# Kernel tuning notes

Hardware: AMD Instinct MI355X
Metric: run time of the kernel (lower is better)

The kernel has to match this reference:

```python
import jax, jax.numpy as jnp
import numpy as np

B, T, D = 4, 2048, 1024
N_HEADS = 16
D_HEAD = D // N_HEADS


def setup_inputs() -> dict:
    key = jax.random.key(0)
    ks = jax.random.split(key, 5)
    s = 1.0 / np.sqrt(D)
    return {
        "x": jax.random.normal(ks[0], (B, T, D), dtype=jnp.float32),
        "wq": jax.random.normal(ks[1], (D, D), dtype=jnp.float32) * s,
        "wk": jax.random.normal(ks[2], (D, D), dtype=jnp.float32) * s,
        "wv": jax.random.normal(ks[3], (D, D), dtype=jnp.float32) * s,
        "wo": jax.random.normal(ks[4], (D, D), dtype=jnp.float32) * s,
    }


def reference(x, wq, wk, wv, wo):
    # nn.Linear applies y = x @ W^T (no bias)
    b, t, c = x.shape
    def heads(w):
        return (x @ w.T).reshape(b, t, N_HEADS, D_HEAD).transpose(0, 2, 1, 3)  # (B,H,T,d)
    q, k, v = heads(wq), heads(wk), heads(wv)
    scale = 1.0 / np.sqrt(D_HEAD).astype(np.float32)
    att = jnp.einsum('bhqd,bhkd->bhqk', q, k) * scale
    causal = jnp.tril(jnp.ones((t, t), dtype=bool))
    att = jnp.where(causal[None, None], att, -jnp.inf)
    att = jax.nn.softmax(att, axis=-1)
    # dropout is identity in eval / p acts as 0 for the deterministic reference
    y = jnp.einsum('bhqk,bhkd->bhqd', att, v)
    y = y.transpose(0, 2, 1, 3).reshape(b, t, c)
    return y @ wo.T
```

## Files before the change

### kernel.cpp

```cpp
#include <hip/hip_runtime.h>

#define B_ 4
#define T_ 2048
#define D_ 1024
#define H_ 16
#define DH_ 64
#define M_ (B_*T_)
#define KP 72

typedef __attribute__((ext_vector_type(8))) short short8;
typedef __attribute__((ext_vector_type(4))) float f32x4;
typedef __attribute__((ext_vector_type(4))) unsigned short u16x4;
typedef _Float16 half4f __attribute__((ext_vector_type(4)));

__device__ __forceinline__ unsigned short f2bf(float f) {
  unsigned int u = __float_as_uint(f);
  u += 0x7FFFu + ((u >> 16) & 1u);
  return (unsigned short)(u >> 16);
}

__device__ __forceinline__ void async_copy16(const void* g, void* l) {
  __builtin_amdgcn_global_load_lds(
      (const __attribute__((address_space(1))) unsigned int*)(g),
      (__attribute__((address_space(3))) unsigned int*)(l),
      16, 0, 0);
}

__device__ __forceinline__ f32x4 mfma32(short8 a, short8 b, f32x4 c) {
  return __builtin_amdgcn_mfma_f32_16x16x32_bf16(a, b, c, 0, 0, 0);
}

#define NX4 (M_*D_/4)
#define NW4 (D_*D_/4)
__global__ __launch_bounds__(256) void cvt_all(
    const float* __restrict__ x,  const float* __restrict__ wq,
    const float* __restrict__ wk, const float* __restrict__ wv,
    const float* __restrict__ wo, unsigned short* __restrict__ xb,
    unsigned short* __restrict__ wqb, unsigned short* __restrict__ wkb,
    unsigned short* __restrict__ wvb, unsigned short* __restrict__ wob) {
  int i = blockIdx.x * 256 + threadIdx.x;
  const float* src; unsigned short* dst; int off;
  if (i < NX4)             { src = x;  dst = xb;  off = i; }
  else if (i < NX4 + NW4)  { src = wq; dst = wqb; off = i - NX4; }
  else if (i < NX4 + 2*NW4){ src = wk; dst = wkb; off = i - NX4 - NW4; }
  else if (i < NX4 + 3*NW4){ src = wv; dst = wvb; off = i - NX4 - 2*NW4; }
  else                     { src = wo; dst = wob; off = i - NX4 - 3*NW4; }
  const float4 v = reinterpret_cast<const float4*>(src)[off];
  u16x4 o;
  o.x = f2bf(v.x); o.y = f2bf(v.y); o.z = f2bf(v.z); o.w = f2bf(v.w);
  reinterpret_cast<u16x4*>(dst)[off] = o;
}

__global__ __launch_bounds__(256) void gemm_qkv(
    const unsigned short* __restrict__ A,
    const unsigned short* __restrict__ Wq,
    const unsigned short* __restrict__ Wk,
    const unsigned short* __restrict__ Wv,
    unsigned short* __restrict__ Qo,
    unsigned short* __restrict__ Ko,
    _Float16* __restrict__ Vo) {
  __shared__ __align__(16) unsigned short ldsA[128*32];
  __shared__ __align__(16) unsigned short ldsB[128*32];
  const int tid = threadIdx.x;
  const int w = tid >> 6, lane = tid & 63;
  const int quad = lane >> 4, l16 = lane & 15;
  const int wr = (w >> 1) * 64, wc = (w & 1) * 64;
  const int m0 = blockIdx.x * 128;
  const int seg = blockIdx.y >> 3;
  const int n0 = (blockIdx.y & 7) * 128;
  const unsigned short* Bt = (seg == 0) ? Wq : ((seg == 1) ? Wk : Wv);

  const unsigned short* gA = A  + (size_t)(m0 + w*32 + (lane >> 2)) * D_ + (lane & 3) * 8;
  const unsigned short* gB = Bt + (size_t)(n0 + w*32 + (lane >> 2)) * D_ + (lane & 3) * 8;
  unsigned short* lA = ldsA + (w*32)*32;
  unsigned short* lB = ldsB + (w*32)*32;

  f32x4 acc[4][4] = {};

  for (int k0 = 0; k0 < D_; k0 += 32) {
    __syncthreads();
#pragma unroll
    for (int g = 0; g < 2; ++g) {
      async_copy16(gA + (size_t)k0 + (size_t)g*16*D_, lA + g*16*32);
      async_copy16(gB + (size_t)k0 + (size_t)g*16*D_, lB + g*16*32);
    }
    __syncthreads();
    short8 af[4], bfr[4];
#pragma unroll
    for (int t = 0; t < 4; ++t) {
      af[t]  = *reinterpret_cast<const short8*>(ldsA + (wr + t*16 + l16)*32 + quad*8);
      bfr[t] = *reinterpret_cast<const short8*>(ldsB + (wc + t*16 + l16)*32 + quad*8);
    }
#pragma unroll
    for (int i = 0; i < 4; ++i)
#pragma unroll
      for (int j = 0; j < 4; ++j)
        acc[i][j] = mfma32(af[i], bfr[j], acc[i][j]);
  }

#pragma unroll
  for (int i = 0; i < 4; ++i) {
#pragma unroll
    for (int j = 0; j < 4; ++j) {
      if (seg == 2) {
        const int colc = n0 + wc + j*16 + l16;
        const int hh = colc >> 6, dd = colc & (DH_ - 1);
        const int row0 = m0 + wr + i*16 + quad*4;
        const int bb = row0 >> 11, t0 = row0 & (T_ - 1);
        half4f vh = {(_Float16)acc[i][j][0], (_Float16)acc[i][j][1],
                     (_Float16)acc[i][j][2], (_Float16)acc[i][j][3]};
        *reinterpret_cast<half4f*>(
            &Vo[(size_t)((bb*H_ + hh)*DH_ + dd)*T_ + t0]) = vh;
      } else {
        unsigned short* out = (seg == 0) ? Qo : Ko;
        const float scl = (seg == 0) ? (0.125f * 1.44269504089f) : 1.f;
#pragma unroll
        for (int r = 0; r < 4; ++r) {
          const int row = m0 + wr + i*16 + quad*4 + r;
          const int col = n0 + wc + j*16 + l16;
          out[(size_t)row * D_ + col] = f2bf(acc[i][j][r] * scl);
        }
      }
    }
  }
}

__global__ __launch_bounds__(256) void gemm_out(
    const unsigned short* __restrict__ A,
    const unsigned short* __restrict__ Bt,
    float* __restrict__ Cout) {
  __shared__ __align__(16) unsigned short ldsA[128*32];
  __shared__ __align__(16) unsigned short ldsB[128*32];
  const int tid = threadIdx.x;
  const int w = tid >> 6, lane = tid & 63;
  const int quad = lane >> 4, l16 = lane & 15;
  const int wr = (w >> 1) * 64, wc = (w & 1) * 64;
  const int m0 = blockIdx.x * 128, n0 = blockIdx.y * 128;

  const unsigned short* gA = A  + (size_t)(m0 + w*32 + (lane >> 2)) * D_ + (lane & 3) * 8;
  const unsigned short* gB = Bt + (size_t)(n0 + w*32 + (lane >> 2)) * D_ + (lane & 3) * 8;
  unsigned short* lA = ldsA + (w*32)*32;
  unsigned short* lB = ldsB + (w*32)*32;

  f32x4 acc[4][4] = {};
  for (int k0 = 0; k0 < D_; k0 += 32) {
    __syncthreads();
#pragma unroll
    for (int g = 0; g < 2; ++g) {
      async_copy16(gA + (size_t)k0 + (size_t)g*16*D_, lA + g*16*32);
      async_copy16(gB + (size_t)k0 + (size_t)g*16*D_, lB + g*16*32);
    }
    __syncthreads();
    short8 af[4], bfr[4];
#pragma unroll
    for (int t = 0; t < 4; ++t) {
      af[t]  = *reinterpret_cast<const short8*>(ldsA + (wr + t*16 + l16)*32 + quad*8);
      bfr[t] = *reinterpret_cast<const short8*>(ldsB + (wc + t*16 + l16)*32 + quad*8);
    }
#pragma unroll
    for (int i = 0; i < 4; ++i)
#pragma unroll
      for (int j = 0; j < 4; ++j)
        acc[i][j] = mfma32(af[i], bfr[j], acc[i][j]);
  }
#pragma unroll
  for (int i = 0; i < 4; ++i)
#pragma unroll
    for (int j = 0; j < 4; ++j)
#pragma unroll
      for (int r = 0; r < 4; ++r)
        Cout[(size_t)(m0 + wr + i*16 + quad*4 + r) * D_ + n0 + wc + j*16 + l16] =
            acc[i][j][r];
}

__global__ __launch_bounds__(256) void flash_attn(
    const unsigned short* __restrict__ Q,
    const unsigned short* __restrict__ K,
    const _Float16* __restrict__ Vt,
    unsigned short* __restrict__ Y) {
  __shared__ __align__(16) unsigned short Kl[2][64*KP];
  __shared__ __align__(16) _Float16      Vl[2][64*KP];
  const int bh = blockIdx.x, px = blockIdx.y;
  const int h = bh & (H_ - 1), b = bh >> 4;
  const int tid = threadIdx.x;
  const int w = tid >> 6, lane = tid & 63, quad = lane >> 4, l16 = lane & 15;
  const int hc = h * DH_;

  const int sr = tid >> 2, sc = tid & 3;
  const unsigned short* Kg0 = K + ((size_t)(b*T_) + sr) * D_ + hc + sc*16;
  const _Float16*       Vg0 = Vt + ((size_t)bh * DH_ + sr) * T_ + sc*16;

  uint4 kr0, kr1, vr0, vr1;
  auto loadKV = [&](int kt) {
    const unsigned short* kg = Kg0 + (size_t)kt * 64 * D_;
    const _Float16*       vg = Vg0 + kt * 64;
    kr0 = *reinterpret_cast<const uint4*>(kg);
    kr1 = *reinterpret_cast<const uint4*>(kg + 8);
    vr0 = *reinterpret_cast<const uint4*>(vg);
    vr1 = *reinterpret_cast<const uint4*>(vg + 8);
  };
  auto writeKV = [&](int bi) {
    *reinterpret_cast<uint4*>(&Kl[bi][sr*KP + sc*16])     = kr0;
    *reinterpret_cast<uint4*>(&Kl[bi][sr*KP + sc*16 + 8]) = kr1;
    *reinterpret_cast<uint4*>(&Vl[bi][sr*KP + sc*16])     = vr0;
    *reinterpret_cast<uint4*>(&Vl[bi][sr*KP + sc*16 + 8]) = vr1;
  };

#pragma unroll
  for (int pi = 0; pi < 2; ++pi) {
    const int it = pi ? (31 - px) : px;
    const int qg0 = it*64 + w*16;

    short8 bq[2];
#pragma unroll
    for (int ks = 0; ks < 2; ++ks)
      bq[ks] = *reinterpret_cast<const short8*>(
          Q + (size_t)(b*T_ + qg0 + l16) * D_ + hc + ks*32 + quad*8);

    f32x4 o[4] = {};
    float rs = 0.f;
    const int ktmax = it;

    __syncthreads();
    loadKV(0);
    writeKV(0);
    __syncthreads();

    for (int kt = 0; kt <= ktmax; ++kt) {
      const int cur = kt & 1;
      if (kt < ktmax) loadKV(kt + 1);
      const bool diag = (kt == ktmax);
      const int smax = diag ? w : 3;
      const int diagS = diag ? w : -1;
      for (int s = 0; s <= smax; ++s) {
        const short8 ka0 = *reinterpret_cast<const short8*>(
            &Kl[cur][(s*16 + l16)*KP + quad*8]);
        const short8 ka1 = *reinterpret_cast<const short8*>(
            &Kl[cur][(s*16 + l16)*KP + 32 + quad*8]);
        f32x4 z = {0.f, 0.f, 0.f, 0.f};
        z = mfma32(ka0, bq[0], z);
        z = mfma32(ka1, bq[1], z);
        float p[4];
        const bool dsub = (s == diagS);
#pragma unroll
        for (int r = 0; r < 4; ++r) {
          float pv = __builtin_amdgcn_exp2f(z[r]);
          if (dsub && (quad*4 + r > l16)) pv = 0.f;
          p[r] = pv;
          rs += pv;
        }
        const half4f pf = {(_Float16)p[0], (_Float16)p[1],
                           (_Float16)p[2], (_Float16)p[3]};
#pragma unroll
        for (int dt = 0; dt < 4; ++dt) {
          const half4f vf = *reinterpret_cast<const half4f*>(
              &Vl[cur][(dt*16 + l16)*KP + s*16 + quad*4]);
          o[dt] = __builtin_amdgcn_mfma_f32_16x16x16f16(vf, pf, o[dt], 0, 0, 0);
        }
      }
      if (kt < ktmax) {
        __syncthreads();
        writeKV(cur ^ 1);
        __syncthreads();
      }
    }

    float rt = rs;
    rt += __shfl_xor(rt, 16);
    rt += __shfl_xor(rt, 32);
    const float inv = 1.f / rt;

#pragma unroll
    for (int dt = 0; dt < 4; ++dt) {
      u16x4 yo;
      yo.x = f2bf(o[dt][0] * inv);
      yo.y = f2bf(o[dt][1] * inv);
      yo.z = f2bf(o[dt][2] * inv);
      yo.w = f2bf(o[dt][3] * inv);
      *reinterpret_cast<u16x4*>(
          &Y[(size_t)(b*T_ + qg0 + l16) * D_ + hc + dt*16 + quad*4]) = yo;
    }
  }
}

extern "C" void kernel_launch(void* const* d_in, const int* in_sizes, int n_in,
                              void* d_out, int out_size, void* d_ws, size_t ws_size,
                              hipStream_t stream) {
  const float* x  = (const float*)d_in[0];
  const float* wq = (const float*)d_in[1];
  const float* wk = (const float*)d_in[2];
  const float* wv = (const float*)d_in[3];
  const float* wo = (const float*)d_in[4];

  unsigned short* xb  = (unsigned short*)d_ws;
  unsigned short* wqb = xb  + (size_t)M_ * D_;
  unsigned short* wkb = wqb + (size_t)D_ * D_;
  unsigned short* wvb = wkb + (size_t)D_ * D_;
  unsigned short* wob = wvb + (size_t)D_ * D_;
  unsigned short* q   = wob + (size_t)D_ * D_;
  unsigned short* k   = q   + (size_t)M_ * D_;
  _Float16*       vt  = (_Float16*)(k + (size_t)M_ * D_);
  unsigned short* y   = (unsigned short*)(vt + (size_t)M_ * D_);

  const int ncv = (NX4 + 4*NW4 + 255) / 256;
  cvt_all<<<ncv, 256, 0, stream>>>(x, wq, wk, wv, wo, xb, wqb, wkb, wvb, wob);

  gemm_qkv<<<dim3(M_ / 128, 24), 256, 0, stream>>>(xb, wqb, wkb, wvb, q, k, vt);

  flash_attn<<<dim3(64, 16), 256, 0, stream>>>(q, k, vt, y);

  gemm_out<<<dim3(M_ / 128, D_ / 128), 256, 0, stream>>>(y, wob, (float*)d_out);
}
```

Before: 252.5 us.

## Process both paired query tiles in one KV sweep sharing K/V loads

After: 245.1 us. 2.9% less time.

```diff
diff --git a/kernel.cpp b/kernel.cpp
--- a/kernel.cpp
+++ b/kernel.cpp
@@ -12,6 +12,7 @@
 typedef __attribute__((ext_vector_type(4))) float f32x4;
 typedef __attribute__((ext_vector_type(4))) unsigned short u16x4;
 typedef _Float16 half4f __attribute__((ext_vector_type(4)));
+typedef __fp16 h2raw __attribute__((ext_vector_type(2)));
 
 __device__ __forceinline__ unsigned short f2bf(float f) {
   unsigned int u = __float_as_uint(f);
@@ -28,6 +29,9 @@
 
 __device__ __forceinline__ f32x4 mfma32(short8 a, short8 b, f32x4 c) {
   return __builtin_amdgcn_mfma_f32_16x16x32_bf16(a, b, c, 0, 0, 0);
+}
+__device__ __forceinline__ f32x4 mfma16h(half4f a, half4f b, f32x4 c) {
+  return __builtin_amdgcn_mfma_f32_16x16x16f16(a, b, c, 0, 0, 0);
 }
 
 #define NX4 (M_*D_/4)
@@ -173,7 +177,31 @@
             acc[i][j][r];
 }
 
-__global__ __launch_bounds__(256) void flash_attn(
+__device__ __forceinline__ half4f score_exp(short8 ka0, short8 ka1,
+                                            short8 bq0, short8 bq1,
+                                            bool dmask, int kvb, int qrel,
+                                            f32x4* osum, half4f vones) {
+  f32x4 z = {0.f, 0.f, 0.f, 0.f};
+  z = mfma32(ka0, bq0, z);
+  z = mfma32(ka1, bq1, z);
+  float p0 = __builtin_amdgcn_exp2f(z[0]);
+  float p1 = __builtin_amdgcn_exp2f(z[1]);
+  float p2 = __builtin_amdgcn_exp2f(z[2]);
+  float p3 = __builtin_amdgcn_exp2f(z[3]);
+  if (dmask) {
+    if (kvb + 0 > qrel) p0 = 0.f;
+    if (kvb + 1 > qrel) p1 = 0.f;
+    if (kvb + 2 > qrel) p2 = 0.f;
+    if (kvb + 3 > qrel) p3 = 0.f;
+  }
+  union { h2raw h2[2]; half4f h4; } u;
+  u.h2[0] = __builtin_amdgcn_cvt_pkrtz(p0, p1);
+  u.h2[1] = __builtin_amdgcn_cvt_pkrtz(p2, p3);
+  *osum = mfma16h(vones, u.h4, *osum);
+  return u.h4;
+}
+
+__global__ __launch_bounds__(256, 4) void flash_attn(
     const unsigned short* __restrict__ Q,
     const unsigned short* __restrict__ K,
     const _Float16* __restrict__ Vt,
@@ -185,6 +213,9 @@
   const int tid = threadIdx.x;
   const int w = tid >> 6, lane = tid & 63, quad = lane >> 4, l16 = lane & 15;
   const int hc = h * DH_;
+  const int itA = px, itB = 31 - px;
+  const int qgA = itA*64 + w*16, qgB = itB*64 + w*16;
+  const int ktmax = itB;
 
   const int sr = tid >> 2, sc = tid & 3;
   const unsigned short* Kg0 = K + ((size_t)(b*T_) + sr) * D_ + hc + sc*16;
@@ -206,80 +237,69 @@
     *reinterpret_cast<uint4*>(&Vl[bi][sr*KP + sc*16 + 8]) = vr1;
   };
 
-#pragma unroll
-  for (int pi = 0; pi < 2; ++pi) {
-    const int it = pi ? (31 - px) : px;
-    const int qg0 = it*64 + w*16;
-
-    short8 bq[2];
-#pragma unroll
-    for (int ks = 0; ks < 2; ++ks)
-      bq[ks] = *reinterpret_cast<const short8*>(
-          Q + (size_t)(b*T_ + qg0 + l16) * D_ + hc + ks*32 + quad*8);
-
-    f32x4 o[4] = {};
-    float rs = 0.f;
-    const int ktmax = it;
-
-    __syncthreads();
-    loadKV(0);
-    writeKV(0);
-    __syncthreads();
-
-    for (int kt = 0; kt <= ktmax; ++kt) {
-      const int cur = kt & 1;
-      if (kt < ktmax) loadKV(kt + 1);
-      const bool diag = (kt == ktmax);
-      const int smax = diag ? w : 3;
-      const int diagS = diag ? w : -1;
-      for (int s = 0; s <= smax; ++s) {
-        const short8 ka0 = *reinterpret_cast<const short8*>(
-            &Kl[cur][(s*16 + l16)*KP + quad*8]);
-        const short8 ka1 = *reinterpret_cast<const short8*>(
-            &Kl[cur][(s*16 + l16)*KP + 32 + quad*8]);
-        f32x4 z = {0.f, 0.f, 0.f, 0.f};
-        z = mfma32(ka0, bq[0], z);
-        z = mfma32(ka1, bq[1], z);
-        float p[4];
-        const bool dsub = (s == diagS);
-#pragma unroll
-        for (int r = 0; r < 4; ++r) {
-          float pv = __builtin_amdgcn_exp2f(z[r]);
-          if (dsub && (quad*4 + r > l16)) pv = 0.f;
-          p[r] = pv;
-          rs += pv;
-        }
-        const half4f pf = {(_Float16)p[0], (_Float16)p[1],
-                           (_Float16)p[2], (_Float16)p[3]};
-#pragma unroll
-        for (int dt = 0; dt < 4; ++dt) {
-          const half4f vf = *reinterpret_cast<const half4f*>(
-              &Vl[cur][(dt*16 + l16)*KP + s*16 + quad*4]);
-          o[dt] = __builtin_amdgcn_mfma_f32_16x16x16f16(vf, pf, o[dt], 0, 0, 0);
-        }
+  short8 bqA0, bqA1, bqB0, bqB1;
+  bqA0 = *reinterpret_cast<const short8*>(
+      Q + (size_t)(b*T_ + qgA + l16) * D_ + hc + quad*8);
+  bqA1 = *reinterpret_cast<const short8*>(
+      Q + (size_t)(b*T_ + qgA + l16) * D_ + hc + 32 + quad*8);
+  bqB0 = *reinterpret_cast<const short8*>(
+      Q + (size_t)(b*T_ + qgB + l16) * D_ + hc + quad*8);
+  bqB1 = *reinterpret_cast<const short8*>(
+      Q + (size_t)(b*T_ + qgB + l16) * D_ + hc + 32 + quad*8);
+
+  f32x4 oA[4] = {}, oB[4] = {};
+  f32x4 osA = {}, osB = {};
+  const half4f vones = {(_Float16)1.f, (_Float16)1.f, (_Float16)1.f, (_Float16)1.f};
+  const int qrelW = w*16 + l16;
+
+  loadKV(0);
+  writeKV(0);
+  __syncthreads();
+
+  for (int kt = 0; kt <= ktmax; ++kt) {
+    const int cur = kt & 1;
+    if (kt < ktmax) loadKV(kt + 1);
+    const bool aOn   = (kt <= px);
+    const bool aDiag = (kt == px);
+    const bool bDiag = (kt == ktmax);
+    const int smax = bDiag ? w : 3;
+    for (int s = 0; s <= smax; ++s) {
+      const short8 ka0 = *reinterpret_cast<const short8*>(
+          &Kl[cur][(s*16 + l16)*KP + quad*8]);
+      const short8 ka1 = *reinterpret_cast<const short8*>(
+          &Kl[cur][(s*16 + l16)*KP + 32 + quad*8]);
+      const int kvb = s*16 + quad*4;
+      half4f pfA;
+      if (aOn) pfA = score_exp(ka0, ka1, bqA0, bqA1, aDiag, kvb, qrelW, &osA, vones);
+      const half4f pfB = score_exp(ka0, ka1, bqB0, bqB1, bDiag, kvb, qrelW, &osB, vones);
+#pragma unroll
+      for (int dt = 0; dt < 4; ++dt) {
+        const half4f vf = *reinterpret_cast<const half4f*>(
+            &Vl[cur][(dt*16 + l16)*KP + s*16 + quad*4]);
+        if (aOn) oA[dt] = mfma16h(vf, pfA, oA[dt]);
+        oB[dt] = mfma16h(vf, pfB, oB[dt]);
       }
-      if (kt < ktmax) {
-        __syncthreads();
-        writeKV(cur ^ 1);
-        __syncthreads();
-      }
-    }
-
-    float rt = rs;
-    rt += __shfl_xor(rt, 16);
-    rt += __shfl_xor(rt, 32);
-    const float inv = 1.f / rt;
-
-#pragma unroll
-    for (int dt = 0; dt < 4; ++dt) {
-      u16x4 yo;
-      yo.x = f2bf(o[dt][0] * inv);
-      yo.y = f2bf(o[dt][1] * inv);
-      yo.z = f2bf(o[dt][2] * inv);
-      yo.w = f2bf(o[dt][3] * inv);
-      *reinterpret_cast<u16x4*>(
-          &Y[(size_t)(b*T_ + qg0 + l16) * D_ + hc + dt*16 + quad*4]) = yo;
-    }
+    }
+    if (kt < ktmax) {
+      __syncthreads();
+      writeKV(cur ^ 1);
+      __syncthreads();
+    }
+  }
+
+  const float invA = 1.f / osA[0];
+  const float invB = 1.f / osB[0];
+#pragma unroll
+  for (int dt = 0; dt < 4; ++dt) {
+    u16x4 ya, yb;
+    ya.x = f2bf(oA[dt][0] * invA); ya.y = f2bf(oA[dt][1] * invA);
+    ya.z = f2bf(oA[dt][2] * invA); ya.w = f2bf(oA[dt][3] * invA);
+    yb.x = f2bf(oB[dt][0] * invB); yb.y = f2bf(oB[dt][1] * invB);
+    yb.z = f2bf(oB[dt][2] * invB); yb.w = f2bf(oB[dt][3] * invB);
+    *reinterpret_cast<u16x4*>(
+        &Y[(size_t)(b*T_ + qgA + l16) * D_ + hc + dt*16 + quad*4]) = ya;
+    *reinterpret_cast<u16x4*>(
+        &Y[(size_t)(b*T_ + qgB + l16) * D_ + hc + dt*16 + quad*4]) = yb;
   }
 }
 
```
